# Performance work log

Measured on AMD Instinct MI355X. Metric: run time of the kernel, lower is better.

The kernel has to match this reference:

```python
import jax, jax.numpy as jnp
import numpy as np

N = 50000        # nodes
E = 800000       # edges (avg degree 16)
DIN = 256        # input feature dim
D = 128          # embedding_dim
B = 8            # graphs in batch
ITERS = 2        # num_iterations


def setup_inputs() -> dict:
    key = jax.random.key(0)
    ks = jax.random.split(key, 16)
    w = lambda k, shape: jax.random.normal(k, shape, jnp.float32) * 0.05
    z = lambda n: jnp.zeros((n,), jnp.float32)
    return {
        "nodes": jax.random.normal(ks[0], (N, DIN), jnp.float32),
        "edges": jax.random.randint(ks[1], (2, E), 0, N),
        "batch": jnp.sort(jax.random.randint(ks[2], (N,), 0, B)),
        # initial encoder Linear(DIN, D)
        "W_enc": w(ks[3], (DIN, D)), "b_enc": z(D),
        # parent aggregation MLP: Linear(2D, D) -> ReLU -> Linear(D, D)
        "Wp1": w(ks[4], (2 * D, D)), "bp1": z(D),
        "Wp2": w(ks[5], (D, D)), "bp2": z(D),
        # child aggregation MLP
        "Wc1": w(ks[6], (2 * D, D)), "bc1": z(D),
        "Wc2": w(ks[7], (D, D)), "bc2": z(D),
        # final agg: Linear(3D, 2D) -> ReLU -> Linear(2D, D)
        "Wf1": w(ks[8], (3 * D, 2 * D)), "bf1": z(2 * D),
        "Wf2": w(ks[9], (2 * D, D)), "bf2": z(D),
        # Conv1d(D, 2D, kernel=1) == Linear(D, 2D)
        "Wconv": w(ks[10], (D, 2 * D)), "bconv": z(2 * D),
    }


def _edge_agg(x, idx_i, idx_j, W1, b1, W2, b2, inv_deg):
    # message: mlp(cat(x_i, x_j)); scatter-sum at idx_i; degree-normalize.
    h = jnp.concatenate([x[idx_i], x[idx_j]], axis=1)         # [E, 2D]
    m = jax.nn.relu(h @ W1 + b1) @ W2 + b2                    # [E, D]
    agg = jax.ops.segment_sum(m, idx_i, num_segments=x.shape[0])
    return agg * inv_deg[:, None]


def reference(nodes, edges, batch, W_enc, b_enc, Wp1, bp1, Wp2, bp2,
              Wc1, bc1, Wc2, bc2, Wf1, bf1, Wf2, bf2, Wconv, bconv):
    src, dst = edges[0], edges[1]
    ones_e = jnp.ones((edges.shape[1],), nodes.dtype)
    deg_dst = jax.ops.segment_sum(ones_e, dst, num_segments=N)
    deg_src = jax.ops.segment_sum(ones_e, src, num_segments=N)
    inv_dst = jnp.where(deg_dst > 0, 1.0 / deg_dst, 0.0)
    inv_src = jnp.where(deg_src > 0, 1.0 / deg_src, 0.0)

    x = nodes @ W_enc + b_enc                                  # [N, D]
    for _ in range(ITERS):
        # Parent_Aggregation: x_i = x[dst], x_j = x[src], sum at dst, / in-deg
        fi = _edge_agg(x, dst, src, Wp1, bp1, Wp2, bp2, inv_dst)
        # Child_Aggregation:  x_i = x[src], x_j = x[dst], sum at src, / out-deg
        fo = _edge_agg(x, src, dst, Wc1, bc1, Wc2, bc2, inv_src)
        h = jnp.concatenate([x, fi, fo], axis=1)               # [N, 3D]
        x = x + (jax.nn.relu(h @ Wf1 + bf1) @ Wf2 + bf2)

    y = x @ Wconv + bconv                                      # conv1d k=1 -> [N, 2D]
    gmax = jax.ops.segment_max(y, batch, num_segments=B)       # global_max_pool
    cnt = jax.ops.segment_sum(jnp.ones((N,), y.dtype), batch, num_segments=B)
    gmean = jax.ops.segment_sum(y, batch, num_segments=B) / cnt[:, None]
    return jnp.concatenate([gmax, gmean], axis=1)              # [B, 4D]
```

## Files before the change

kernel.cpp:

```cpp
#include <hip/hip_runtime.h>
#include <hip/hip_bf16.h>
#include <float.h>

typedef __hip_bfloat16 bf16;
typedef short short8 __attribute__((ext_vector_type(8)));
typedef short short4v __attribute__((ext_vector_type(4)));
typedef float f32x4 __attribute__((ext_vector_type(4)));
typedef unsigned short u16;
typedef unsigned char u8;

__device__ __forceinline__ float toF(bf16 v) { return __bfloat162float(v); }
__device__ __forceinline__ float s2f(short s) {
    return __uint_as_float(((unsigned int)(unsigned short)s) << 16);
}
__device__ __forceinline__ short f2s(float f) {
    bf16 h = __float2bfloat16(f);
    return *(short*)&h;
}

__global__ void diag_kernel(float* __restrict__ out, float v, int n) {
    int i = blockIdx.x * 256 + threadIdx.x;
    if (i < n) out[i] = v;
}

__global__ void init_kernel(int* __restrict__ deg2, float* __restrict__ cnt_gsum,
                            float* __restrict__ gmax, int* __restrict__ flag, int n2) {
    int i = blockIdx.x * 256 + threadIdx.x;
    if (i < n2) deg2[i] = 0;
    if (i < 8 + 2048) cnt_gsum[i] = 0.f;
    if (i < 2048) gmax[i] = -FLT_MAX;
    if (i == 0) *flag = 1;
}

__global__ void probe_kernel(const unsigned int* __restrict__ w, int nwords,
                             int* __restrict__ flag) {
    int i = blockIdx.x * 256 + threadIdx.x;
    bool bad = false;
    if (i < nwords) {
        float v = __uint_as_float((w[i] & 0xFFFFu) << 16);
        bad = !(v > -1e3f && v < 1e3f);
    }
    if (__any(bad) && (threadIdx.x & 63) == 0) atomicAnd(flag, 0);
}

struct M1 {
    const int* edges; int E;
    int* degd; int* degs; u8* rankd; u8* ranks;
    const int* batch; int Nn; float* cnt;
    const void* wsrc[10]; int woff[10]; bf16* wdst[10];
    int wK[10]; int wNC[10]; int wstart[11];
    const void* bsrc[8]; bf16* bdst[8]; int bn[8];
    const void* nsrc; bf16* ndst; int nElems;
    const int* flag;
    int sCnt, sSwz, sBias, sConv;
};

__global__ void mega1_kernel(M1 a) {
    int b = blockIdx.x, tid = threadIdx.x;
    if (b < a.sCnt) {
        const int* es = a.edges;
        const int* ed = a.edges + a.E;
        int e0 = (b * 256 + tid) * 4;
        if (e0 + 4 <= a.E) {
            int4 s4 = *(const int4*)(es + e0);
            int4 d4 = *(const int4*)(ed + e0);
            uchar4 rs, rd;
            rs.x = (u8)atomicAdd(&a.degs[s4.x], 1);
            rs.y = (u8)atomicAdd(&a.degs[s4.y], 1);
            rs.z = (u8)atomicAdd(&a.degs[s4.z], 1);
            rs.w = (u8)atomicAdd(&a.degs[s4.w], 1);
            rd.x = (u8)atomicAdd(&a.degd[d4.x], 1);
            rd.y = (u8)atomicAdd(&a.degd[d4.y], 1);
            rd.z = (u8)atomicAdd(&a.degd[d4.z], 1);
            rd.w = (u8)atomicAdd(&a.degd[d4.w], 1);
            *(uchar4*)(a.ranks + e0) = rs;
            *(uchar4*)(a.rankd + e0) = rd;
        } else {
            for (int e = e0; e < a.E; ++e) {
                a.ranks[e] = (u8)atomicAdd(&a.degs[es[e]], 1);
                a.rankd[e] = (u8)atomicAdd(&a.degd[ed[e]], 1);
            }
        }
    } else if (b < a.sSwz) {
        __shared__ float loc[8];
        if (tid < 8) loc[tid] = 0.f;
        __syncthreads();
        int i = (b - a.sCnt) * 256 + tid;
        if (i < a.Nn) atomicAdd(&loc[a.batch[i]], 1.0f);
        __syncthreads();
        if (tid < 8 && loc[tid] > 0.f) atomicAdd(&a.cnt[tid], loc[tid]);
    } else if (b < a.sBias) {
        int bb = b - a.sSwz;
        int seg = 0;
#pragma unroll
        for (int t = 1; t < 10; ++t) if (bb >= a.wstart[t]) seg = t;
        int i = (bb - a.wstart[seg]) * 256 + tid;
        int K = a.wK[seg], NC = a.wNC[seg];
        if (i < K * NC) {
            int KF = K >> 5;
            int j = i & 7;
            int ln = (i >> 3) & 63;
            int q = i >> 9;
            int kb = q % KF;
            int t = q / KF;
            int k = kb * 32 + (ln >> 4) * 8 + j;
            int n = t * 16 + (ln & 15);
            int idx = a.woff[seg] + k * NC + n;
            a.wdst[seg][i] = (*a.flag)
                ? ((const bf16*)a.wsrc[seg])[idx]
                : __float2bfloat16(((const float*)a.wsrc[seg])[idx]);
        }
    } else if (b < a.sConv) {
#pragma unroll
        for (int t = 0; t < 8; ++t)
            for (int i = tid; i < a.bn[t]; i += 256)
                a.bdst[t][i] = (*a.flag)
                    ? ((const bf16*)a.bsrc[t])[i]
                    : __float2bfloat16(((const float*)a.bsrc[t])[i]);
    } else {
        if (*a.flag) return;
        int i = (b - a.sConv) * 2048 + tid * 8;
        if (i + 8 <= a.nElems) {
            const float* f = (const float*)a.nsrc + i;
            short8 o;
#pragma unroll
            for (int j = 0; j < 8; ++j) o[j] = f2s(f[j]);
            *(short8*)((short*)a.ndst + i) = o;
        } else {
            int e = a.nElems;
            for (int jj = i; jj < e && jj < i + 8; ++jj)
                a.ndst[jj] = __float2bfloat16(((const float*)a.nsrc)[jj]);
        }
    }
}

__device__ __forceinline__ void atomicMaxF(float* addr, float val) {
    unsigned int* ua = (unsigned int*)addr;
    unsigned int old = __float_as_uint(*addr);
    while (__uint_as_float(old) < val) {
        unsigned int assumed = old;
        old = atomicCAS(ua, assumed, __float_as_uint(val));
        if (old == assumed) break;
    }
}

template<int K, int NC> struct SB {
    static constexpr int APAD = K + 8;
    static constexpr int CPAD = NC + 8;
    static constexpr int AB = 64 * APAD * 2;
    static constexpr int CB = 64 * CPAD * 2;
    static constexpr int S = AB > CB ? AB : CB;
};

template<int K, int NC, int NSRC, bool RELU, bool RES, bool SCALE, bool POOL, bool STORE>
__device__ __forceinline__ void gemm_core(int bx,
    const bf16* A0, const bf16* A1, const bf16* A2,
    const bf16* WS, const bf16* bias, const float* scale, bf16* C, int M,
    const int* batch, float* gmax, float* gsum, char* smem) {
    constexpr int KF = K / 32;
    constexpr int NH = NC / 128;
    constexpr int APAD = SB<K, NC>::APAD;
    constexpr int CPAD = SB<K, NC>::CPAD;
    short* sA = (short*)smem;

    int tid = threadIdx.x;
    int m0blk = bx * 64;

    constexpr int C8 = K / 8;
    for (int idx = tid; idx < 64 * C8; idx += 256) {
        int r = idx / C8, c8 = idx % C8;
        int row = m0blk + r; row = row < M ? row : M - 1;
        const bf16* src;
        int off;
        if (NSRC == 1) { src = A0; off = c8 * 8; }
        else {
            int seg = c8 >> 4;
            src = seg == 0 ? A0 : (seg == 1 ? A1 : A2);
            off = (c8 & 15) * 8;
        }
        const size_t rs = (NSRC == 1) ? (size_t)K : (size_t)128;
        *(short8*)(sA + r * APAD + c8 * 8) = *(const short8*)((const short*)src + (size_t)row * rs + off);
    }
    __syncthreads();

    int wv = tid >> 6, ln = tid & 63;
    int quad = ln >> 4, ncol = ln & 15;
    int mw = wv * 16;

    short8 a[KF];
#pragma unroll
    for (int kb = 0; kb < KF; ++kb)
        a[kb] = *(const short8*)(sA + (mw + ncol) * APAD + kb * 32 + quad * 8);
    __syncthreads();

    float scl[4];
    if (SCALE) {
#pragma unroll
        for (int r = 0; r < 4; ++r) {
            int orow = m0blk + mw + quad * 4 + r;
            scl[r] = scale[orow < M ? orow : M - 1];
        }
    }

    short* sC = (short*)smem;
    const short8* wsp = (const short8*)WS;
#pragma unroll
    for (int h = 0; h < NH; ++h) {
        f32x4 acc[8];
#pragma unroll
        for (int t = 0; t < 8; ++t) acc[t] = (f32x4){0.f, 0.f, 0.f, 0.f};
        short8 bcur[8], bnxt[8];
#pragma unroll
        for (int t = 0; t < 8; ++t)
            bcur[t] = wsp[(size_t)((h * 8 + t) * KF) * 64 + ln];
#pragma unroll
        for (int kb = 0; kb < KF; ++kb) {
            if (kb + 1 < KF) {
#pragma unroll
                for (int t = 0; t < 8; ++t)
                    bnxt[t] = wsp[(size_t)((h * 8 + t) * KF + kb + 1) * 64 + ln];
            }
#pragma unroll
            for (int t = 0; t < 8; ++t)
                acc[t] = __builtin_amdgcn_mfma_f32_16x16x32_bf16(a[kb], bcur[t], acc[t], 0, 0, 0);
#pragma unroll
            for (int t = 0; t < 8; ++t) bcur[t] = bnxt[t];
        }
#pragma unroll
        for (int t = 0; t < 8; ++t) {
            float bv = bias ? toF(bias[h * 128 + t * 16 + ncol]) : 0.f;
#pragma unroll
            for (int r = 0; r < 4; ++r) {
                float v = acc[t][r];
                if (SCALE) { v *= scl[r]; if (scl[r] > 0.f) v += bv; }
                else v += bv;
                if (RELU) v = fmaxf(v, 0.f);
                sC[(mw + quad * 4 + r) * CPAD + h * 128 + t * 16 + ncol] = f2s(v);
            }
        }
    }
    __syncthreads();
    if (!STORE && !POOL) return;

    if (POOL) {
        int* bs = (int*)(smem + SB<K, NC>::S);
        if (tid < 64) {
            int row = m0blk + tid;
            bs[tid] = (row < M) ? batch[row] : -1;
        }
        __syncthreads();
        int cur_b = -1;
        float mx = -FLT_MAX, sm = 0.f;
        for (int r = 0; r < 64; ++r) {
            int b = bs[r];
            if (b < 0) break;
            float v = s2f(sC[r * CPAD + tid]);
            if (b != cur_b) {
                if (cur_b >= 0) {
                    atomicMaxF(&gmax[cur_b * 256 + tid], mx);
                    atomicAdd(&gsum[cur_b * 256 + tid], sm);
                }
                cur_b = b; mx = v; sm = v;
            } else {
                mx = fmaxf(mx, v);
                sm += v;
            }
        }
        if (cur_b >= 0) {
            atomicMaxF(&gmax[cur_b * 256 + tid], mx);
            atomicAdd(&gsum[cur_b * 256 + tid], sm);
        }
    } else {
        constexpr int OC8 = NC / 8;
        for (int idx = tid; idx < 64 * OC8; idx += 256) {
            int r = idx / OC8, c8 = idx % OC8;
            int row = m0blk + r;
            if (row < M) {
                short8 v = *(short8*)(sC + r * CPAD + c8 * 8);
                size_t o = (size_t)row * NC + c8 * 8;
                if (RES) {
                    short8 old = *(const short8*)((const short*)C + o);
#pragma unroll
                    for (int j = 0; j < 8; ++j) v[j] = f2s(s2f(v[j]) + s2f(old[j]));
                }
                *(short8*)((short*)C + o) = v;
            }
        }
    }
}

template<int K, int NC, int NSRC, bool RELU, bool RES, bool SCALE, bool POOL>
__global__ __launch_bounds__(256, 2)
void gemm_mfma_kernel(const bf16* A0, const bf16* A1, const bf16* A2,
                      const bf16* WS, const bf16* bias,
                      const float* scale, bf16* C, int M,
                      const int* batch, float* gmax, float* gsum) {
    __shared__ __align__(16) char smem[SB<K, NC>::S + (POOL ? 256 : 0)];
    gemm_core<K, NC, NSRC, RELU, RES, SCALE, POOL, true>(
        blockIdx.x, A0, A1, A2, WS, bias, scale, C, M, batch, gmax, gsum, smem);
}

__global__ __launch_bounds__(256, 2)
void sei_kernel(const int* __restrict__ edges, int E,
                const u8* __restrict__ rankd, const u8* __restrict__ ranks,
                u16* __restrict__ adjd, u16* __restrict__ adjs, int CAP,
                const void* nodes_raw, const bf16* Tn, const int* flag,
                const bf16* WSenc, const bf16* benc, bf16* x, int M,
                const int* degd, const int* degs,
                float* invd, float* invs, int gsc, int gb) {
    __shared__ __align__(16) char smem[SB<256, 128>::S];
    int b = blockIdx.x, tid = threadIdx.x;
    if (b < gsc) {
        int e0 = (b * 256 + tid) * 4;
        if (e0 + 4 <= E) {
            int4 s4 = *(const int4*)(edges + e0);
            int4 d4 = *(const int4*)(edges + E + e0);
            uchar4 rs = *(const uchar4*)(ranks + e0);
            uchar4 rd = *(const uchar4*)(rankd + e0);
            if (rs.x < CAP) adjs[s4.x * CAP + rs.x] = (u16)d4.x;
            if (rs.y < CAP) adjs[s4.y * CAP + rs.y] = (u16)d4.y;
            if (rs.z < CAP) adjs[s4.z * CAP + rs.z] = (u16)d4.z;
            if (rs.w < CAP) adjs[s4.w * CAP + rs.w] = (u16)d4.w;
            if (rd.x < CAP) adjd[d4.x * CAP + rd.x] = (u16)s4.x;
            if (rd.y < CAP) adjd[d4.y * CAP + rd.y] = (u16)s4.y;
            if (rd.z < CAP) adjd[d4.z * CAP + rd.z] = (u16)s4.z;
            if (rd.w < CAP) adjd[d4.w * CAP + rd.w] = (u16)s4.w;
        } else {
            for (int e = e0; e < E; ++e) {
                int s_ = edges[e], d_ = edges[E + e];
                if (ranks[e] < CAP) adjs[s_ * CAP + ranks[e]] = (u16)d_;
                if (rankd[e] < CAP) adjd[d_ * CAP + rankd[e]] = (u16)s_;
            }
        }
    } else if (b < gsc + gb) {
        const bf16* A0 = (*flag) ? (const bf16*)nodes_raw : Tn;
        gemm_core<256, 128, 1, false, false, false, false, true>(
            b - gsc, A0, nullptr, nullptr, WSenc, benc, nullptr, x, M,
            nullptr, nullptr, nullptr, smem);
    } else {
        int i = (b - gsc - gb) * 256 + tid;
        if (i < M) {
            int dd = degd[i]; invd[i] = dd > 0 ? 1.0f / (float)dd : 0.0f;
            int ds = degs[i]; invs[i] = ds > 0 ? 1.0f / (float)ds : 0.0f;
        }
    }
}

__device__ __forceinline__ void agg_body(int node, int tid,
        const int* __restrict__ deg, const u16* __restrict__ adj, int CAP,
        const short* __restrict__ PQ, int stride,
        const short* __restrict__ b1, bf16* __restrict__ S) {
    int ln = tid & 63;
    int c4 = ln & 31, half = ln >> 5;
    float p[4];
    {
        short4v pv = *(const short4v*)(PQ + (size_t)node * stride + 4 * c4);
        short4v bv = *(const short4v*)(b1 + 4 * c4);
#pragma unroll
        for (int r = 0; r < 4; ++r) p[r] = s2f(pv[r]) + s2f(bv[r]);
    }
    float a[4] = {0.f, 0.f, 0.f, 0.f};
    int d = deg[node]; d = d < CAP ? d : CAP;
    const u16* ap = adj + (size_t)node * CAP;
    const short* Qb = PQ + 128 + 4 * c4;
    int k = half;
    for (; k + 14 < d; k += 16) {
        int j0 = ap[k],      j1 = ap[k + 2],  j2 = ap[k + 4],  j3 = ap[k + 6];
        int j4 = ap[k + 8],  j5 = ap[k + 10], j6 = ap[k + 12], j7 = ap[k + 14];
        short4v q0 = *(const short4v*)(Qb + (size_t)j0 * stride);
        short4v q1 = *(const short4v*)(Qb + (size_t)j1 * stride);
        short4v q2 = *(const short4v*)(Qb + (size_t)j2 * stride);
        short4v q3 = *(const short4v*)(Qb + (size_t)j3 * stride);
        short4v q4 = *(const short4v*)(Qb + (size_t)j4 * stride);
        short4v q5 = *(const short4v*)(Qb + (size_t)j5 * stride);
        short4v q6 = *(const short4v*)(Qb + (size_t)j6 * stride);
        short4v q7 = *(const short4v*)(Qb + (size_t)j7 * stride);
#pragma unroll
        for (int r = 0; r < 4; ++r)
            a[r] += fmaxf(p[r] + s2f(q0[r]), 0.f) + fmaxf(p[r] + s2f(q1[r]), 0.f)
                  + fmaxf(p[r] + s2f(q2[r]), 0.f) + fmaxf(p[r] + s2f(q3[r]), 0.f)
                  + fmaxf(p[r] + s2f(q4[r]), 0.f) + fmaxf(p[r] + s2f(q5[r]), 0.f)
                  + fmaxf(p[r] + s2f(q6[r]), 0.f) + fmaxf(p[r] + s2f(q7[r]), 0.f);
    }
    for (; k + 6 < d; k += 8) {
        int j0 = ap[k], j1 = ap[k + 2], j2 = ap[k + 4], j3 = ap[k + 6];
        short4v q0 = *(const short4v*)(Qb + (size_t)j0 * stride);
        short4v q1 = *(const short4v*)(Qb + (size_t)j1 * stride);
        short4v q2 = *(const short4v*)(Qb + (size_t)j2 * stride);
        short4v q3 = *(const short4v*)(Qb + (size_t)j3 * stride);
#pragma unroll
        for (int r = 0; r < 4; ++r)
            a[r] += fmaxf(p[r] + s2f(q0[r]), 0.f) + fmaxf(p[r] + s2f(q1[r]), 0.f)
                  + fmaxf(p[r] + s2f(q2[r]), 0.f) + fmaxf(p[r] + s2f(q3[r]), 0.f);
    }
    for (; k < d; k += 2) {
        int j = ap[k];
        short4v q = *(const short4v*)(Qb + (size_t)j * stride);
#pragma unroll
        for (int r = 0; r < 4; ++r) a[r] += fmaxf(p[r] + s2f(q[r]), 0.f);
    }
#pragma unroll
    for (int r = 0; r < 4; ++r) a[r] += __shfl_xor(a[r], 32);
    if (half == 0) {
        short4v o;
#pragma unroll
        for (int r = 0; r < 4; ++r) o[r] = f2s(a[r]);
        *(short4v*)((short*)S + (size_t)node * 128 + 4 * c4) = o;
    }
}

__global__ void agg_kernel(const int* deg, const u16* adj, int CAP,
                           const bf16* PQ, int stride, const bf16* b1,
                           bf16* S, int M) {
    int node = blockIdx.x * 4 + (threadIdx.x >> 6);
    if (node >= M) return;
    agg_body(node, threadIdx.x, deg, adj, CAP, (const short*)PQ, stride,
             (const short*)b1, S);
}

__global__ void agg2_kernel(const int* degd, const u16* adjd,
                            const int* degs, const u16* adjs, int CAP,
                            const bf16* T, const bf16* b1p, const bf16* b1c,
                            bf16* Sd, bf16* Ss, int M, int ga) {
    int b = blockIdx.x, wv = threadIdx.x >> 6;
    if (b < ga) {
        int node = b * 4 + wv;
        if (node < M)
            agg_body(node, threadIdx.x, degd, adjd, CAP, (const short*)T, 512,
                     (const short*)b1p, Sd);
    } else {
        int node = (b - ga) * 4 + wv;
        if (node < M)
            agg_body(node, threadIdx.x, degs, adjs, CAP, (const short*)T + 256, 512,
                     (const short*)b1c, Ss);
    }
}

template<bool FINAL>
__global__ __launch_bounds__(256, 2)
void mega_mlp_kernel(const bf16* __restrict__ x, const bf16* Sd, const bf16* Ss,
                     const bf16* WS2p, const bf16* b2p, const float* invd,
                     const bf16* WS2c, const bf16* b2c, const float* invs,
                     const bf16* WSf1, const bf16* bf1_,
                     const bf16* WSf2, const bf16* bf2_,
                     bf16* xio, int M,
                     const bf16* WSconv, const bf16* bconv,
                     const int* batch, float* gmax, float* gsum) {
    __shared__ __align__(16) char smem[52224 + 256];
    constexpr int RB = 17408;
    short* sm = (short*)smem;
    int tid = threadIdx.x;
    int m0blk = blockIdx.x * 64;

    for (int idx = tid; idx < 64 * 16; idx += 256) {
        int r = idx >> 4, c8 = idx & 15;
        int row = m0blk + r; row = row < M ? row : M - 1;
        *(short8*)(sm + r * 136 + c8 * 8) =
            *(const short8*)((const short*)x + (size_t)row * 128 + c8 * 8);
    }
    gemm_core<128, 128, 1, false, false, true, false, false>(
        blockIdx.x, Sd, nullptr, nullptr, WS2p, b2p, invd, nullptr, M,
        nullptr, nullptr, nullptr, smem + RB);
    gemm_core<128, 128, 1, false, false, true, false, false>(
        blockIdx.x, Ss, nullptr, nullptr, WS2c, b2c, invs, nullptr, M,
        nullptr, nullptr, nullptr, smem + 2 * RB);

    int wv = tid >> 6, ln = tid & 63;
    int quad = ln >> 4, ncol = ln & 15;
    int mw = wv * 16;

    short8 a1[12];
#pragma unroll
    for (int kb = 0; kb < 12; ++kb) {
        const short* sb = sm + (kb >> 2) * (RB / 2);
        a1[kb] = *(const short8*)(sb + (mw + ncol) * 136 + (kb & 3) * 32 + quad * 8);
    }
    __syncthreads();

    short* sH = sm + RB / 2;
    const short8* w1 = (const short8*)WSf1;
#pragma unroll
    for (int h = 0; h < 2; ++h) {
        f32x4 acc[8];
#pragma unroll
        for (int t = 0; t < 8; ++t) acc[t] = (f32x4){0.f, 0.f, 0.f, 0.f};
        short8 bcur[8], bnxt[8];
#pragma unroll
        for (int t = 0; t < 8; ++t)
            bcur[t] = w1[(size_t)((h * 8 + t) * 12) * 64 + ln];
#pragma unroll
        for (int kb = 0; kb < 12; ++kb) {
            if (kb + 1 < 12) {
#pragma unroll
                for (int t = 0; t < 8; ++t)
                    bnxt[t] = w1[(size_t)((h * 8 + t) * 12 + kb + 1) * 64 + ln];
            }
#pragma unroll
            for (int t = 0; t < 8; ++t)
                acc[t] = __builtin_amdgcn_mfma_f32_16x16x32_bf16(a1[kb], bcur[t], acc[t], 0, 0, 0);
#pragma unroll
            for (int t = 0; t < 8; ++t) bcur[t] = bnxt[t];
        }
#pragma unroll
        for (int t = 0; t < 8; ++t) {
            float bv = toF(bf1_[h * 128 + t * 16 + ncol]);
#pragma unroll
            for (int r = 0; r < 4; ++r)
                sH[(mw + quad * 4 + r) * 264 + h * 128 + t * 16 + ncol] =
                    f2s(fmaxf(acc[t][r] + bv, 0.f));
        }
    }
    __syncthreads();

    short8 a2[8];
#pragma unroll
    for (int kb = 0; kb < 8; ++kb)
        a2[kb] = *(const short8*)(sH + (mw + ncol) * 264 + kb * 32 + quad * 8);
    __syncthreads();

    f32x4 acc2[8];
#pragma unroll
    for (int t = 0; t < 8; ++t) acc2[t] = (f32x4){0.f, 0.f, 0.f, 0.f};
    const short8* w2 = (const short8*)WSf2;
    {
        short8 bcur[8], bnxt[8];
#pragma unroll
        for (int t = 0; t < 8; ++t) bcur[t] = w2[(size_t)(t * 8) * 64 + ln];
#pragma unroll
        for (int kb = 0; kb < 8; ++kb) {
            if (kb + 1 < 8) {
#pragma unroll
                for (int t = 0; t < 8; ++t)
                    bnxt[t] = w2[(size_t)(t * 8 + kb + 1) * 64 + ln];
            }
#pragma unroll
            for (int t = 0; t < 8; ++t)
                acc2[t] = __builtin_amdgcn_mfma_f32_16x16x32_bf16(a2[kb], bcur[t], acc2[t], 0, 0, 0);
#pragma unroll
            for (int t = 0; t < 8; ++t) bcur[t] = bnxt[t];
        }
    }
    short* sC2 = sm + RB / 2;
#pragma unroll
    for (int t = 0; t < 8; ++t) {
        float bv = toF(bf2_[t * 16 + ncol]);
#pragma unroll
        for (int r = 0; r < 4; ++r)
            sC2[(mw + quad * 4 + r) * 136 + t * 16 + ncol] = f2s(acc2[t][r] + bv);
    }
    __syncthreads();

    for (int idx = tid; idx < 64 * 16; idx += 256) {
        int r = idx >> 4, c8 = idx & 15;
        short8 v = *(short8*)(sC2 + r * 136 + c8 * 8);
        short8 old = *(const short8*)(sm + r * 136 + c8 * 8);
#pragma unroll
        for (int j = 0; j < 8; ++j) v[j] = f2s(s2f(v[j]) + s2f(old[j]));
        if (FINAL) {
            *(short8*)(sC2 + r * 136 + c8 * 8) = v;
        } else {
            int row = m0blk + r;
            if (row < M) *(short8*)((short*)xio + (size_t)row * 128 + c8 * 8) = v;
        }
    }
    if (!FINAL) return;
    __syncthreads();

    short8 a3[4];
#pragma unroll
    for (int kb = 0; kb < 4; ++kb)
        a3[kb] = *(const short8*)(sC2 + (mw + ncol) * 136 + kb * 32 + quad * 8);
    __syncthreads();

    short* sCc = sm;
    const short8* wc = (const short8*)WSconv;
#pragma unroll
    for (int h = 0; h < 2; ++h) {
        f32x4 acc[8];
#pragma unroll
        for (int t = 0; t < 8; ++t) acc[t] = (f32x4){0.f, 0.f, 0.f, 0.f};
        short8 bcur[8], bnxt[8];
#pragma unroll
        for (int t = 0; t < 8; ++t)
            bcur[t] = wc[(size_t)((h * 8 + t) * 4) * 64 + ln];
#pragma unroll
        for (int kb = 0; kb < 4; ++kb) {
            if (kb + 1 < 4) {
#pragma unroll
                for (int t = 0; t < 8; ++t)
                    bnxt[t] = wc[(size_t)((h * 8 + t) * 4 + kb + 1) * 64 + ln];
            }
#pragma unroll
            for (int t = 0; t < 8; ++t)
                acc[t] = __builtin_amdgcn_mfma_f32_16x16x32_bf16(a3[kb], bcur[t], acc[t], 0, 0, 0);
#pragma unroll
            for (int t = 0; t < 8; ++t) bcur[t] = bnxt[t];
        }
#pragma unroll
        for (int t = 0; t < 8; ++t) {
            float bv = toF(bconv[h * 128 + t * 16 + ncol]);
#pragma unroll
            for (int r = 0; r < 4; ++r)
                sCc[(mw + quad * 4 + r) * 264 + h * 128 + t * 16 + ncol] =
                    f2s(acc[t][r] + bv);
        }
    }
    __syncthreads();

    int* bs = (int*)(smem + 52224);
    if (tid < 64) {
        int row = m0blk + tid;
        bs[tid] = (row < M) ? batch[row] : -1;
    }
    __syncthreads();
    int cur_b = -1;
    float mx = -FLT_MAX, sum_ = 0.f;
    for (int r = 0; r < 64; ++r) {
        int b = bs[r];
        if (b < 0) break;
        float v = s2f(sCc[r * 264 + tid]);
        if (b != cur_b) {
            if (cur_b >= 0) {
                atomicMaxF(&gmax[cur_b * 256 + tid], mx);
                atomicAdd(&gsum[cur_b * 256 + tid], sum_);
            }
            cur_b = b; mx = v; sum_ = v;
        } else {
            mx = fmaxf(mx, v);
            sum_ += v;
        }
    }
    if (cur_b >= 0) {
        atomicMaxF(&gmax[cur_b * 256 + tid], mx);
        atomicAdd(&gsum[cur_b * 256 + tid], sum_);
    }
}

__global__ void out_kernel(const float* __restrict__ gmax, const float* __restrict__ gsum,
                           const float* __restrict__ cnt, const int* __restrict__ flag,
                           void* __restrict__ out) {
    int i = blockIdx.x * 256 + threadIdx.x;
    if (i < 8 * 512) {
        int b = i >> 9, c = i & 511;
        float v = (c < 256) ? gmax[b * 256 + c] : gsum[b * 256 + (c - 256)] / cnt[b];
        int f = *flag;
        if (!(v == v)) v = 1000.f + 100.f * (float)f;
        if (f) ((bf16*)out)[i] = __float2bfloat16(v);
        else   ((float*)out)[i] = v;
    }
}

extern "C" void kernel_launch(void* const* d_in, const int* in_sizes, int n_in,
                              void* d_out, int out_size, void* d_ws, size_t ws_size,
                              hipStream_t stream) {
    const int* edges = (const int*)d_in[1];
    const int* batch = (const int*)d_in[2];

    const int N_ = in_sizes[2];
    const int E_ = in_sizes[1] / 2;
    const size_t ND = (size_t)N_ * 128;

    char* p = (char*)d_ws;
    bf16* x  = (bf16*)p;      p += ND * 2;
    bf16* Sd = (bf16*)p;      p += ND * 2;
    bf16* Ss = (bf16*)p;      p += ND * 2;
    bf16* bias[8];
    for (int t = 0; t < 8; ++t) { bias[t] = (bf16*)p; p += 512 * 2; }
    bf16* WSenc   = (bf16*)p; p += 256 * 128 * 2;
    bf16* WSpqall = (bf16*)p; p += 4 * 128 * 128 * 2;
    bf16* WS2p    = (bf16*)p; p += 128 * 128 * 2;
    bf16* WS2c    = (bf16*)p; p += 128 * 128 * 2;
    bf16* WSf1    = (bf16*)p; p += 384 * 256 * 2;
    bf16* WSf2    = (bf16*)p; p += 256 * 128 * 2;
    bf16* WSconv  = (bf16*)p; p += 128 * 256 * 2;
    int* degd    = (int*)p;   p += (size_t)N_ * 4;
    int* degs    = (int*)p;   p += (size_t)N_ * 4;
    float* invd  = (float*)p; p += (size_t)N_ * 4;
    float* invs  = (float*)p; p += (size_t)N_ * 4;
    float* cnt   = (float*)p; p += 8 * 4;
    float* gsum  = (float*)p; p += 2048 * 4;
    float* gmax  = (float*)p; p += 2048 * 4;
    int* flag    = (int*)p;   p += 64;
    u8* rankd    = (u8*)p;    p += ((size_t)E_ + 15) & ~(size_t)15;
    u8* ranks    = (u8*)p;    p += ((size_t)E_ + 15) & ~(size_t)15;

    size_t used = (size_t)(p - (char*)d_ws);
    size_t rem = ws_size > used ? ws_size - used : 0;
    int CAP = 0, wide = 0;
    if (N_ < 65536) {
        if      (rem >= (size_t)2 * N_ * 64 * 2 + (size_t)N_ * 512 * 2) { CAP = 64; wide = 1; }
        else if (rem >= (size_t)2 * N_ * 64 * 2 + (size_t)N_ * 256 * 2) { CAP = 64; wide = 0; }
        else if (rem >= (size_t)2 * N_ * 48 * 2 + (size_t)N_ * 256 * 2) { CAP = 48; wide = 0; }
    }
    if (!CAP) {
        diag_kernel<<<(out_size + 255) / 256, 256, 0, stream>>>((float*)d_out, (float)(ws_size >> 20), out_size);
        return;
    }
    u16* adjd = (u16*)p;      p += (size_t)N_ * CAP * 2;
    u16* adjs = (u16*)p;      p += (size_t)N_ * CAP * 2;
    bf16* T   = (bf16*)p;

    int gN  = (N_ + 255) / 256;
    int gE4 = (E_ + 1023) / 1024;
    int gb  = (N_ + 63) / 64;
    int ga  = (N_ + 3) / 4;

    init_kernel<<<(2 * N_ + 255) / 256, 256, 0, stream>>>(degd, cnt, gmax, flag, 2 * N_);
    probe_kernel<<<8, 256, 0, stream>>>((const unsigned int*)d_in[3], 2048, flag);

    M1 a;
    a.edges = edges; a.E = E_;
    a.degd = degd; a.degs = degs; a.rankd = rankd; a.ranks = ranks;
    a.batch = batch; a.Nn = N_; a.cnt = cnt;
    a.nsrc = d_in[0]; a.ndst = T; a.nElems = in_sizes[0];
    {
        const int bidx[8] = {4, 6, 8, 10, 12, 14, 16, 18};
        for (int t = 0; t < 8; ++t) {
            a.bsrc[t] = d_in[bidx[t]];
            a.bdst[t] = bias[t];
            a.bn[t] = in_sizes[bidx[t]];
        }
        const void* wraw[10] = {d_in[3], d_in[5], d_in[5], d_in[9], d_in[9],
                                d_in[7], d_in[11], d_in[13], d_in[15], d_in[17]};
        int woff[10]  = {0, 0, 128 * 128, 0, 128 * 128, 0, 0, 0, 0, 0};
        bf16* wdst[10] = {WSenc, WSpqall, WSpqall + 16384, WSpqall + 32768, WSpqall + 49152,
                          WS2p, WS2c, WSf1, WSf2, WSconv};
        int wK[10]  = {256, 128, 128, 128, 128, 128, 128, 384, 256, 128};
        int wNC[10] = {128, 128, 128, 128, 128, 128, 128, 256, 128, 256};
        int wb_ = 0;
        for (int t = 0; t < 10; ++t) {
            a.wsrc[t] = wraw[t]; a.woff[t] = woff[t]; a.wdst[t] = wdst[t];
            a.wK[t] = wK[t]; a.wNC[t] = wNC[t];
            a.wstart[t] = wb_;
            wb_ += (wK[t] * wNC[t] + 255) / 256;
        }
        a.wstart[10] = wb_;
        a.flag = flag;
        a.sCnt  = gE4;
        a.sSwz  = a.sCnt + gN;
        a.sBias = a.sSwz + wb_;
        a.sConv = a.sBias + 1;
        int convB = (a.nElems + 2047) / 2048;
        mega1_kernel<<<a.sConv + convB, 256, 0, stream>>>(a);
    }

    sei_kernel<<<gE4 + gb + gN, 256, 0, stream>>>(
        edges, E_, rankd, ranks, adjd, adjs, CAP,
        d_in[0], T, flag, WSenc, bias[0], x, N_,
        degd, degs, invd, invs, gE4, gb);

    for (int it = 0; it < 2; ++it) {
        if (wide) {
            gemm_mfma_kernel<128, 512, 1, false, false, false, false><<<gb, 256, 0, stream>>>(
                x, nullptr, nullptr, WSpqall, nullptr, nullptr, T, N_, nullptr, nullptr, nullptr);
            agg2_kernel<<<2 * ga, 256, 0, stream>>>(degd, adjd, degs, adjs, CAP,
                                                    T, bias[1], bias[3], Sd, Ss, N_, ga);
        } else {
            gemm_mfma_kernel<128, 256, 1, false, false, false, false><<<gb, 256, 0, stream>>>(
                x, nullptr, nullptr, WSpqall, nullptr, nullptr, T, N_, nullptr, nullptr, nullptr);
            agg_kernel<<<ga, 256, 0, stream>>>(degd, adjd, CAP, T, 256, bias[1], Sd, N_);
            gemm_mfma_kernel<128, 256, 1, false, false, false, false><<<gb, 256, 0, stream>>>(
                x, nullptr, nullptr, WSpqall + 32768, nullptr, nullptr, T, N_, nullptr, nullptr, nullptr);
            agg_kernel<<<ga, 256, 0, stream>>>(degs, adjs, CAP, T, 256, bias[3], Ss, N_);
        }
        if (it == 0)
            mega_mlp_kernel<false><<<gb, 256, 0, stream>>>(
                x, Sd, Ss, WS2p, bias[2], invd, WS2c, bias[4], invs,
                WSf1, bias[5], WSf2, bias[6], x, N_,
                WSconv, bias[7], batch, gmax, gsum);
        else
            mega_mlp_kernel<true><<<gb, 256, 0, stream>>>(
                x, Sd, Ss, WS2p, bias[2], invd, WS2c, bias[4], invs,
                WSf1, bias[5], WSf2, bias[6], x, N_,
                WSconv, bias[7], batch, gmax, gsum);
    }

    out_kernel<<<16, 256, 0, stream>>>(gmax, gsum, cnt, flag, d_out);
}
```

Before: 626.9 us.

## Fold second-layer message weights into final MLP weights algebraically

Because segment-sum and degree normalization are linear, the second Linear of each edge MLP is folded into Wf1: the kernel precomputes W2p·Wf1 and W2c·Wf1 blocks plus bias terms (b2·Wf1), applied only where a node's degree is positive. The two per-iteration 128x128 GEMMs in the mega MLP kernel are removed, and degree scaling moves into the aggregation epilogue. This adds a small weight-precompute stage to the setup kernel. The folded products are rounded to bf16, which changes rounding compared with the two-step path.

```diff
diff --git a/kernel.cpp b/kernel.cpp
--- a/kernel.cpp
+++ b/kernel.cpp
@@ -16,6 +16,9 @@
 __device__ __forceinline__ short f2s(float f) {
     bf16 h = __float2bfloat16(f);
     return *(short*)&h;
+}
+__device__ __forceinline__ float rdw(const void* p, int i, int f) {
+    return f ? toF(((const bf16*)p)[i]) : ((const float*)p)[i];
 }
 
 __global__ void diag_kernel(float* __restrict__ out, float v, int n) {
@@ -47,12 +50,15 @@
     const int* edges; int E;
     int* degd; int* degs; u8* rankd; u8* ranks;
     const int* batch; int Nn; float* cnt;
-    const void* wsrc[10]; int woff[10]; bf16* wdst[10];
-    int wK[10]; int wNC[10]; int wstart[11];
+    const void* wsrc[7]; int woff[7]; bf16* wdst[7];
+    int wK[7]; int wNC[7]; int wstart[8];
     const void* bsrc[8]; bf16* bdst[8]; int bn[8];
     const void* nsrc; bf16* ndst; int nElems;
+    const void* w2praw; const void* w2craw; const void* wf1raw;
+    const void* b2praw; const void* b2craw;
+    bf16* wsf1; bf16* ub; bf16* vb;
     const int* flag;
-    int sCnt, sSwz, sBias, sConv;
+    int sCnt, sSwz, sBias, sConv, sFw, sUv;
 };
 
 __global__ void mega1_kernel(M1 a) {
@@ -93,7 +99,7 @@
         int bb = b - a.sSwz;
         int seg = 0;
 #pragma unroll
-        for (int t = 1; t < 10; ++t) if (bb >= a.wstart[t]) seg = t;
+        for (int t = 1; t < 7; ++t) if (bb >= a.wstart[t]) seg = t;
         int i = (bb - a.wstart[seg]) * 256 + tid;
         int K = a.wK[seg], NC = a.wNC[seg];
         if (i < K * NC) {
@@ -117,7 +123,7 @@
                 a.bdst[t][i] = (*a.flag)
                     ? ((const bf16*)a.bsrc[t])[i]
                     : __float2bfloat16(((const float*)a.bsrc[t])[i]);
-    } else {
+    } else if (b < a.sFw) {
         if (*a.flag) return;
         int i = (b - a.sConv) * 2048 + tid * 8;
         if (i + 8 <= a.nElems) {
@@ -130,6 +136,40 @@
             int e = a.nElems;
             for (int jj = i; jj < e && jj < i + 8; ++jj)
                 a.ndst[jj] = __float2bfloat16(((const float*)a.nsrc)[jj]);
+        }
+    } else if (b < a.sUv) {
+        int i = (b - a.sFw) * 256 + tid;
+        int j = i & 7;
+        int ln = (i >> 3) & 63;
+        int q = i >> 9;
+        int kb = q % 12;
+        int t = q / 12;
+        int k = kb * 32 + (ln >> 4) * 8 + j;
+        int n = t * 16 + (ln & 15);
+        int f = *a.flag;
+        float val;
+        if (k < 128) {
+            val = rdw(a.wf1raw, k * 256 + n, f);
+        } else {
+            const void* w2 = (k < 256) ? a.w2praw : a.w2craw;
+            int arow = k & 127;
+            int base = (k < 256) ? 128 : 256;
+            float s = 0.f;
+            for (int c = 0; c < 128; ++c)
+                s += rdw(w2, arow * 128 + c, f) * rdw(a.wf1raw, (base + c) * 256 + n, f);
+            val = s;
+        }
+        a.wsf1[i] = __float2bfloat16(val);
+    } else {
+        if (tid < 256) {
+            int f = *a.flag;
+            float su = 0.f, sv = 0.f;
+            for (int c = 0; c < 128; ++c) {
+                su += rdw(a.b2praw, c, f) * rdw(a.wf1raw, (128 + c) * 256 + tid, f);
+                sv += rdw(a.b2craw, c, f) * rdw(a.wf1raw, (256 + c) * 256 + tid, f);
+            }
+            a.ub[tid] = __float2bfloat16(su);
+            a.vb[tid] = __float2bfloat16(sv);
         }
     }
 }
@@ -152,10 +192,10 @@
     static constexpr int S = AB > CB ? AB : CB;
 };
 
-template<int K, int NC, int NSRC, bool RELU, bool RES, bool SCALE, bool POOL, bool STORE>
+template<int K, int NC, int NSRC, bool RELU, bool RES, bool POOL, bool STORE>
 __device__ __forceinline__ void gemm_core(int bx,
     const bf16* A0, const bf16* A1, const bf16* A2,
-    const bf16* WS, const bf16* bias, const float* scale, bf16* C, int M,
+    const bf16* WS, const bf16* bias, bf16* C, int M,
     const int* batch, float* gmax, float* gsum, char* smem) {
     constexpr int KF = K / 32;
     constexpr int NH = NC / 128;
@@ -193,15 +233,6 @@
         a[kb] = *(const short8*)(sA + (mw + ncol) * APAD + kb * 32 + quad * 8);
     __syncthreads();
 
-    float scl[4];
-    if (SCALE) {
-#pragma unroll
-        for (int r = 0; r < 4; ++r) {
-            int orow = m0blk + mw + quad * 4 + r;
-            scl[r] = scale[orow < M ? orow : M - 1];
-        }
-    }
-
     short* sC = (short*)smem;
     const short8* wsp = (const short8*)WS;
 #pragma unroll
@@ -231,9 +262,7 @@
             float bv = bias ? toF(bias[h * 128 + t * 16 + ncol]) : 0.f;
 #pragma unroll
             for (int r = 0; r < 4; ++r) {
-                float v = acc[t][r];
-                if (SCALE) { v *= scl[r]; if (scl[r] > 0.f) v += bv; }
-                else v += bv;
+                float v = acc[t][r] + bv;
                 if (RELU) v = fmaxf(v, 0.f);
                 sC[(mw + quad * 4 + r) * CPAD + h * 128 + t * 16 + ncol] = f2s(v);
             }
@@ -289,15 +318,14 @@
     }
 }
 
-template<int K, int NC, int NSRC, bool RELU, bool RES, bool SCALE, bool POOL>
+template<int K, int NC, int NSRC, bool RELU, bool RES, bool POOL>
 __global__ __launch_bounds__(256, 2)
 void gemm_mfma_kernel(const bf16* A0, const bf16* A1, const bf16* A2,
-                      const bf16* WS, const bf16* bias,
-                      const float* scale, bf16* C, int M,
+                      const bf16* WS, const bf16* bias, bf16* C, int M,
                       const int* batch, float* gmax, float* gsum) {
     __shared__ __align__(16) char smem[SB<K, NC>::S + (POOL ? 256 : 0)];
-    gemm_core<K, NC, NSRC, RELU, RES, SCALE, POOL, true>(
-        blockIdx.x, A0, A1, A2, WS, bias, scale, C, M, batch, gmax, gsum, smem);
+    gemm_core<K, NC, NSRC, RELU, RES, POOL, true>(
+        blockIdx.x, A0, A1, A2, WS, bias, C, M, batch, gmax, gsum, smem);
 }
 
 __global__ __launch_bounds__(256, 2)
@@ -334,8 +362,8 @@
         }
     } else if (b < gsc + gb) {
         const bf16* A0 = (*flag) ? (const bf16*)nodes_raw : Tn;
-        gemm_core<256, 128, 1, false, false, false, false, true>(
-            b - gsc, A0, nullptr, nullptr, WSenc, benc, nullptr, x, M,
+        gemm_core<256, 128, 1, false, false, false, true>(
+            b - gsc, A0, nullptr, nullptr, WSenc, benc, x, M,
             nullptr, nullptr, nullptr, smem);
     } else {
         int i = (b - gsc - gb) * 256 + tid;
@@ -348,6 +376,7 @@
 
 __device__ __forceinline__ void agg_body(int node, int tid,
         const int* __restrict__ deg, const u16* __restrict__ adj, int CAP,
+        const float* __restrict__ inv,
         const short* __restrict__ PQ, int stride,
         const short* __restrict__ b1, bf16* __restrict__ S) {
     int ln = tid & 63;
@@ -361,6 +390,7 @@
     }
     float a[4] = {0.f, 0.f, 0.f, 0.f};
     int d = deg[node]; d = d < CAP ? d : CAP;
+    float invv = inv[node];
     const u16* ap = adj + (size_t)node * CAP;
     const short* Qb = PQ + 128 + 4 * c4;
     int k = half;
@@ -404,34 +434,34 @@
     if (half == 0) {
         short4v o;
 #pragma unroll
-        for (int r = 0; r < 4; ++r) o[r] = f2s(a[r]);
+        for (int r = 0; r < 4; ++r) o[r] = f2s(a[r] * invv);
         *(short4v*)((short*)S + (size_t)node * 128 + 4 * c4) = o;
     }
 }
 
 __global__ void agg_kernel(const int* deg, const u16* adj, int CAP,
-                           const bf16* PQ, int stride, const bf16* b1,
-                           bf16* S, int M) {
+                           const float* inv, const bf16* PQ, int stride,
+                           const bf16* b1, bf16* S, int M) {
     int node = blockIdx.x * 4 + (threadIdx.x >> 6);
     if (node >= M) return;
-    agg_body(node, threadIdx.x, deg, adj, CAP, (const short*)PQ, stride,
+    agg_body(node, threadIdx.x, deg, adj, CAP, inv, (const short*)PQ, stride,
              (const short*)b1, S);
 }
 
-__global__ void agg2_kernel(const int* degd, const u16* adjd,
-                            const int* degs, const u16* adjs, int CAP,
-                            const bf16* T, const bf16* b1p, const bf16* b1c,
+__global__ void agg2_kernel(const int* degd, const u16* adjd, const float* invd,
+                            const int* degs, const u16* adjs, const float* invs,
+                            int CAP, const bf16* T, const bf16* b1p, const bf16* b1c,
                             bf16* Sd, bf16* Ss, int M, int ga) {
     int b = blockIdx.x, wv = threadIdx.x >> 6;
     if (b < ga) {
         int node = b * 4 + wv;
         if (node < M)
-            agg_body(node, threadIdx.x, degd, adjd, CAP, (const short*)T, 512,
+            agg_body(node, threadIdx.x, degd, adjd, CAP, invd, (const short*)T, 512,
                      (const short*)b1p, Sd);
     } else {
         int node = (b - ga) * 4 + wv;
         if (node < M)
-            agg_body(node, threadIdx.x, degs, adjs, CAP, (const short*)T + 256, 512,
+            agg_body(node, threadIdx.x, degs, adjs, CAP, invs, (const short*)T + 256, 512,
                      (const short*)b1c, Ss);
     }
 }
@@ -439,8 +469,8 @@
 template<bool FINAL>
 __global__ __launch_bounds__(256, 2)
 void mega_mlp_kernel(const bf16* __restrict__ x, const bf16* Sd, const bf16* Ss,
-                     const bf16* WS2p, const bf16* b2p, const float* invd,
-                     const bf16* WS2c, const bf16* b2c, const float* invs,
+                     const int* __restrict__ degd, const int* __restrict__ degs,
+                     const bf16* __restrict__ ub, const bf16* __restrict__ vb,
                      const bf16* WSf1, const bf16* bf1_,
                      const bf16* WSf2, const bf16* bf2_,
                      bf16* xio, int M,
@@ -452,18 +482,18 @@
     int tid = threadIdx.x;
     int m0blk = blockIdx.x * 64;
 
-    for (int idx = tid; idx < 64 * 16; idx += 256) {
-        int r = idx >> 4, c8 = idx & 15;
-        int row = m0blk + r; row = row < M ? row : M - 1;
-        *(short8*)(sm + r * 136 + c8 * 8) =
-            *(const short8*)((const short*)x + (size_t)row * 128 + c8 * 8);
-    }
-    gemm_core<128, 128, 1, false, false, true, false, false>(
-        blockIdx.x, Sd, nullptr, nullptr, WS2p, b2p, invd, nullptr, M,
-        nullptr, nullptr, nullptr, smem + RB);
-    gemm_core<128, 128, 1, false, false, true, false, false>(
-        blockIdx.x, Ss, nullptr, nullptr, WS2c, b2c, invs, nullptr, M,
-        nullptr, nullptr, nullptr, smem + 2 * RB);
+#pragma unroll
+    for (int reg = 0; reg < 3; ++reg) {
+        const short* sp = reg == 0 ? (const short*)x
+                        : (reg == 1 ? (const short*)Sd : (const short*)Ss);
+        for (int idx = tid; idx < 64 * 16; idx += 256) {
+            int r = idx >> 4, c8 = idx & 15;
+            int row = m0blk + r; row = row < M ? row : M - 1;
+            *(short8*)(sm + reg * (RB / 2) + r * 136 + c8 * 8) =
+                *(const short8*)(sp + (size_t)row * 128 + c8 * 8);
+        }
+    }
+    __syncthreads();
 
     int wv = tid >> 6, ln = tid & 63;
     int quad = ln >> 4, ncol = ln & 15;
@@ -477,6 +507,14 @@
     }
     __syncthreads();
 
+    bool md[4], ms[4];
+#pragma unroll
+    for (int r = 0; r < 4; ++r) {
+        int orow = m0blk + mw + quad * 4 + r; orow = orow < M ? orow : M - 1;
+        md[r] = degd[orow] > 0;
+        ms[r] = degs[orow] > 0;
+    }
+
     short* sH = sm + RB / 2;
     const short8* w1 = (const short8*)WSf1;
 #pragma unroll
@@ -503,11 +541,15 @@
         }
 #pragma unroll
         for (int t = 0; t < 8; ++t) {
-            float bv = toF(bf1_[h * 128 + t * 16 + ncol]);
-#pragma unroll
-            for (int r = 0; r < 4; ++r)
-                sH[(mw + quad * 4 + r) * 264 + h * 128 + t * 16 + ncol] =
-                    f2s(fmaxf(acc[t][r] + bv, 0.f));
+            int col = h * 128 + t * 16 + ncol;
+            float bv = toF(bf1_[col]);
+            float uu = toF(ub[col]);
+            float vv = toF(vb[col]);
+#pragma unroll
+            for (int r = 0; r < 4; ++r) {
+                float v = acc[t][r] + bv + (md[r] ? uu : 0.f) + (ms[r] ? vv : 0.f);
+                sH[(mw + quad * 4 + r) * 264 + col] = f2s(fmaxf(v, 0.f));
+            }
         }
     }
     __syncthreads();
@@ -666,10 +708,10 @@
     bf16* Ss = (bf16*)p;      p += ND * 2;
     bf16* bias[8];
     for (int t = 0; t < 8; ++t) { bias[t] = (bf16*)p; p += 512 * 2; }
+    bf16* ub      = (bf16*)p; p += 256 * 2;
+    bf16* vb      = (bf16*)p; p += 256 * 2;
     bf16* WSenc   = (bf16*)p; p += 256 * 128 * 2;
     bf16* WSpqall = (bf16*)p; p += 4 * 128 * 128 * 2;
-    bf16* WS2p    = (bf16*)p; p += 128 * 128 * 2;
-    bf16* WS2c    = (bf16*)p; p += 128 * 128 * 2;
     bf16* WSf1    = (bf16*)p; p += 384 * 256 * 2;
     bf16* WSf2    = (bf16*)p; p += 256 * 128 * 2;
     bf16* WSconv  = (bf16*)p; p += 128 * 256 * 2;
@@ -713,6 +755,9 @@
     a.degd = degd; a.degs = degs; a.rankd = rankd; a.ranks = ranks;
     a.batch = batch; a.Nn = N_; a.cnt = cnt;
     a.nsrc = d_in[0]; a.ndst = T; a.nElems = in_sizes[0];
+    a.w2praw = d_in[7]; a.w2craw = d_in[11]; a.wf1raw = d_in[13];
+    a.b2praw = d_in[8]; a.b2craw = d_in[12];
+    a.wsf1 = WSf1; a.ub = ub; a.vb = vb;
     {
         const int bidx[8] = {4, 6, 8, 10, 12, 14, 16, 18};
         for (int t = 0; t < 8; ++t) {
@@ -720,28 +765,30 @@
             a.bdst[t] = bias[t];
             a.bn[t] = in_sizes[bidx[t]];
         }
-        const void* wraw[10] = {d_in[3], d_in[5], d_in[5], d_in[9], d_in[9],
-                                d_in[7], d_in[11], d_in[13], d_in[15], d_in[17]};
-        int woff[10]  = {0, 0, 128 * 128, 0, 128 * 128, 0, 0, 0, 0, 0};
-        bf16* wdst[10] = {WSenc, WSpqall, WSpqall + 16384, WSpqall + 32768, WSpqall + 49152,
-                          WS2p, WS2c, WSf1, WSf2, WSconv};
-        int wK[10]  = {256, 128, 128, 128, 128, 128, 128, 384, 256, 128};
-        int wNC[10] = {128, 128, 128, 128, 128, 128, 128, 256, 128, 256};
+        const void* wraw[7] = {d_in[3], d_in[5], d_in[5], d_in[9], d_in[9],
+                               d_in[15], d_in[17]};
+        int woff[7]  = {0, 0, 128 * 128, 0, 128 * 128, 0, 0};
+        bf16* wdst[7] = {WSenc, WSpqall, WSpqall + 16384, WSpqall + 32768,
+                         WSpqall + 49152, WSf2, WSconv};
+        int wK[7]  = {256, 128, 128, 128, 128, 256, 128};
+        int wNC[7] = {128, 128, 128, 128, 128, 128, 256};
         int wb_ = 0;
-        for (int t = 0; t < 10; ++t) {
+        for (int t = 0; t < 7; ++t) {
             a.wsrc[t] = wraw[t]; a.woff[t] = woff[t]; a.wdst[t] = wdst[t];
             a.wK[t] = wK[t]; a.wNC[t] = wNC[t];
             a.wstart[t] = wb_;
             wb_ += (wK[t] * wNC[t] + 255) / 256;
         }
-        a.wstart[10] = wb_;
+        a.wstart[7] = wb_;
         a.flag = flag;
         a.sCnt  = gE4;
         a.sSwz  = a.sCnt + gN;
         a.sBias = a.sSwz + wb_;
         a.sConv = a.sBias + 1;
         int convB = (a.nElems + 2047) / 2048;
-        mega1_kernel<<<a.sConv + convB, 256, 0, stream>>>(a);
+        a.sFw = a.sConv + convB;
+        a.sUv = a.sFw + 384;
+        mega1_kernel<<<a.sUv + 1, 256, 0, stream>>>(a);
     }
 
     sei_kernel<<<gE4 + gb + gN, 256, 0, stream>>>(
@@ -751,26 +798,26 @@
 
     for (int it = 0; it < 2; ++it) {
         if (wide) {
-            gemm_mfma_kernel<128, 512, 1, false, false, false, false><<<gb, 256, 0, stream>>>(
-                x, nullptr, nullptr, WSpqall, nullptr, nullptr, T, N_, nullptr, nullptr, nullptr);
-            agg2_kernel<<<2 * ga, 256, 0, stream>>>(degd, adjd, degs, adjs, CAP,
-                                                    T, bias[1], bias[3], Sd, Ss, N_, ga);
+            gemm_mfma_kernel<128, 512, 1, false, false, false><<<gb, 256, 0, stream>>>(
+                x, nullptr, nullptr, WSpqall, nullptr, T, N_, nullptr, nullptr, nullptr);
+            agg2_kernel<<<2 * ga, 256, 0, stream>>>(degd, adjd, invd, degs, adjs, invs,
+                                                    CAP, T, bias[1], bias[3], Sd, Ss, N_, ga);
         } else {
-            gemm_mfma_kernel<128, 256, 1, false, false, false, false><<<gb, 256, 0, stream>>>(
-                x, nullptr, nullptr, WSpqall, nullptr, nullptr, T, N_, nullptr, nullptr, nullptr);
-            agg_kernel<<<ga, 256, 0, stream>>>(degd, adjd, CAP, T, 256, bias[1], Sd, N_);
-            gemm_mfma_kernel<128, 256, 1, false, false, false, false><<<gb, 256, 0, stream>>>(
-                x, nullptr, nullptr, WSpqall + 32768, nullptr, nullptr, T, N_, nullptr, nullptr, nullptr);
-            agg_kernel<<<ga, 256, 0, stream>>>(degs, adjs, CAP, T, 256, bias[3], Ss, N_);
+            gemm_mfma_kernel<128, 256, 1, false, false, false><<<gb, 256, 0, stream>>>(
+                x, nullptr, nullptr, WSpqall, nullptr, T, N_, nullptr, nullptr, nullptr);
+            agg_kernel<<<ga, 256, 0, stream>>>(degd, adjd, CAP, invd, T, 256, bias[1], Sd, N_);
+            gemm_mfma_kernel<128, 256, 1, false, false, false><<<gb, 256, 0, stream>>>(
+                x, nullptr, nullptr, WSpqall + 32768, nullptr, T, N_, nullptr, nullptr, nullptr);
+            agg_kernel<<<ga, 256, 0, stream>>>(degs, adjs, CAP, invs, T, 256, bias[3], Ss, N_);
         }
         if (it == 0)
             mega_mlp_kernel<false><<<gb, 256, 0, stream>>>(
-                x, Sd, Ss, WS2p, bias[2], invd, WS2c, bias[4], invs,
+                x, Sd, Ss, degd, degs, ub, vb,
                 WSf1, bias[5], WSf2, bias[6], x, N_,
                 WSconv, bias[7], batch, gmax, gsum);
         else
             mega_mlp_kernel<true><<<gb, 256, 0, stream>>>(
-                x, Sd, Ss, WS2p, bias[2], invd, WS2c, bias[4], invs,
+                x, Sd, Ss, degd, degs, ub, vb,
                 WSf1, bias[5], WSf2, bias[6], x, N_,
                 WSconv, bias[7], batch, gmax, gsum);
     }
```

After: 637.1 us. Within noise of the previous version (+1.6%).
